# Kernel tuning notes

Hardware: AMD Instinct MI355X
Metric: run time of the kernel (lower is better)

## Reference

```python
import jax, jax.numpy as jnp
import numpy as np

GAMMA = 1.0  # matches init_kwargs gamma
B, N, M = 128, 512, 512


def setup_inputs() -> dict:
    key = jax.random.key(0)
    D = jax.random.uniform(key, (B, N, M), dtype=jnp.float32)
    return {"D": D}


def _softmin3(a, b, c, gamma):
    # soft_min over the 3 DP neighbors: -gamma * logsumexp(-x/gamma)
    z = jnp.stack([a, b, c], axis=0) * (-1.0 / gamma)
    return -gamma * jax.nn.logsumexp(z, axis=0)


def reference(D):
    """Soft-DTW forward: returns R[:, N, M], shape (B,).
    DP over rows (lax.scan), inner scan over columns carries R[i, j-1].
    Vectorized over the batch dimension.
    """
    gamma = GAMMA
    b, n, m = D.shape
    dt = D.dtype
    inf = jnp.array(jnp.inf, dt)

    def row_step(prev_row, d_row):
        # prev_row: (b, m+1) = R[i-1, 0..m]; d_row: (b, m) = D[:, i-1, :]
        def col_step(left, xs):
            diag, up, d = xs  # each (b,)
            new = d + _softmin3(diag, up, left, gamma)
            return new, new
        xs = (prev_row[:, :-1].T, prev_row[:, 1:].T, d_row.T)  # each (m, b)
        _, outs = jax.lax.scan(col_step, jnp.full((b,), inf, dt), xs)
        new_row = jnp.concatenate([jnp.full((b, 1), inf, dt), outs.T], axis=1)
        return new_row, None

    # R[0, :] = [0, inf, inf, ...]
    init = jnp.concatenate([jnp.zeros((b, 1), dt), jnp.full((b, m), inf, dt)], axis=1)
    final_row, _ = jax.lax.scan(row_step, init, jnp.swapaxes(D, 0, 1))  # scan over rows (n, b, m)
    return final_row[:, -1]
```

## Files before the change

kernel.cpp:

```cpp
#include <hip/hip_runtime.h>


#define BB 128
#define NN 512
#define MM 512
#define L2E 1.4426950408889634f
#define LN2 0.6931471805599453f

__device__ __forceinline__ int iclamp(int x, int lo, int hi) {
    return x < lo ? lo : (x > hi ? hi : x);
}

template<int CTRL>
__device__ __forceinline__ float dpp_fmax(float v) {
    const int s = __builtin_amdgcn_update_dpp(
        __float_as_int(v), __float_as_int(v), CTRL, 0xF, 0xF, false);
    return __builtin_fmaxf(v, __int_as_float(s));
}

template<int P, int U, bool JCHK>
__device__ __forceinline__ void dostep(
    const float* __restrict__ Db, const int lane, const int w,
    const int jb, const int sbase, const int tq,
    float (&r1)[2], float (&r2)[2], float2 (&buf)[2][8],
    int& irow, float& sh, float& shprev, float& bl, float& bd,
    float (*hs)[2])
{
    {
        const int r = iclamp(irow, 0, NN - 1);
        buf[P ^ 1][U] = *(const float2*)(Db + ((r << 9) + jb));
        irow += 1;
    }

    float nv1;
    {
        constexpr int par  = (U >= 1) ? P : (P ^ 1);
        constexpr int slot = (U >= 1) ? (U - 1) : 7;
        const float d = buf[par][slot].y;
        float wgt = __builtin_amdgcn_exp2f(-L2E * d);
        if (JCHK) {
            const bool junk = (sbase + (P * 8 + U - 1)) >= tq;
            wgt = junk ? 0.0f : wgt;
        }
        nv1 = wgt * ((r1[1] + r1[0]) + r2[0]);
    }
    if (lane == 63) hs[w][U & 1] = nv1;

    float nv0;
    {
        const float lf = (lane == 0) ? bl : sh;
        const float dg = (lane == 0) ? bd : shprev;
        const float d  = buf[P][U].x;
        float wgt = __builtin_amdgcn_exp2f(-L2E * d);
        if (JCHK) {
            const bool junk = (sbase + (P * 8 + U)) >= tq;
            wgt = junk ? 0.0f : wgt;
        }
        nv0 = wgt * ((r1[0] + lf) + dg);
    }

    r2[0] = r1[0]; r2[1] = r1[1];
    r1[0] = nv0;   r1[1] = nv1;
    bd = bl;

    asm volatile("s_waitcnt lgkmcnt(0)" ::: "memory");
    __builtin_amdgcn_s_barrier();
    asm volatile("" ::: "memory");

    shprev = sh;
    sh = __shfl_up(r1[1], 1, 64);
    if (w > 0) bl = hs[w - 1][U & 1];
}

__device__ __forceinline__ void renorm4(
    const int lane, const int w,
    float (&r1)[2], float (&r2)[2], float& sh, float& shprev,
    float& bl, float& bd, float& gexp, float* mxs)
{
    float m = __builtin_fmaxf(r1[0], r1[1]);
    m = dpp_fmax<0x111>(m);
    m = dpp_fmax<0x112>(m);
    m = dpp_fmax<0x114>(m);
    m = dpp_fmax<0x118>(m);
    m = dpp_fmax<0x142>(m);
    m = dpp_fmax<0x143>(m);
    if (lane == 63) mxs[w] = m;
    asm volatile("s_waitcnt lgkmcnt(0)" ::: "memory");
    __builtin_amdgcn_s_barrier();
    asm volatile("" ::: "memory");
    const float m4 = __builtin_fmaxf(__builtin_fmaxf(mxs[0], mxs[1]),
                                     __builtin_fmaxf(mxs[2], mxs[3]));
    const int eb = (__float_as_int(m4) >> 23) & 255;
    const int ex = (eb > 0 && eb < 255) ? (eb - 127) : 0;
    const float rs = __int_as_float((127 - ex) << 23);
    r1[0] *= rs; r1[1] *= rs; r2[0] *= rs; r2[1] *= rs;
    sh *= rs; shprev *= rs;
    bl *= rs;
    bd *= rs;
    gexp += (float)ex;
}

#define S8(PP, JJ) \
    dostep<PP,0,JJ>(Db,lane,w,jb,sbase,tq,r1,r2,buf,irow,sh,shprev,bl,bd,hs); \
    dostep<PP,1,JJ>(Db,lane,w,jb,sbase,tq,r1,r2,buf,irow,sh,shprev,bl,bd,hs); \
    dostep<PP,2,JJ>(Db,lane,w,jb,sbase,tq,r1,r2,buf,irow,sh,shprev,bl,bd,hs); \
    dostep<PP,3,JJ>(Db,lane,w,jb,sbase,tq,r1,r2,buf,irow,sh,shprev,bl,bd,hs); \
    dostep<PP,4,JJ>(Db,lane,w,jb,sbase,tq,r1,r2,buf,irow,sh,shprev,bl,bd,hs); \
    dostep<PP,5,JJ>(Db,lane,w,jb,sbase,tq,r1,r2,buf,irow,sh,shprev,bl,bd,hs); \
    dostep<PP,6,JJ>(Db,lane,w,jb,sbase,tq,r1,r2,buf,irow,sh,shprev,bl,bd,hs); \
    dostep<PP,7,JJ>(Db,lane,w,jb,sbase,tq,r1,r2,buf,irow,sh,shprev,bl,bd,hs);

__launch_bounds__(256, 1)
__global__ void softdtw_wave4(const float* __restrict__ D, float* __restrict__ out) {
    const int b = blockIdx.x;
    const int tid = (int)threadIdx.x;
    const int w = tid >> 6;
    const int lane = tid & 63;
    const int jb = (w << 7) + (lane << 1);
    const int tq = jb + NN;
    const float* __restrict__ Db = D + (size_t)b * (NN * MM);

    __shared__ float hsS[4][2];
    __shared__ float mxsS[4];
    float (*hs)[2] = hsS;
    float* mxs = mxsS;

    if (tid < 8) ((float*)hsS)[tid] = 0.0f;
    if (tid < 4) mxsS[tid] = 0.0f;
    asm volatile("s_waitcnt lgkmcnt(0)" ::: "memory");
    __builtin_amdgcn_s_barrier();
    asm volatile("" ::: "memory");

    float r1[2] = {0.0f, 0.0f};
    float r2[2] = {0.0f, 0.0f};
    float2 buf[2][8];
    #pragma unroll
    for (int v = 0; v < 8; ++v) buf[1][v] = make_float2(0.0f, 0.0f);
    #pragma unroll
    for (int v = 0; v < 8; ++v) {
        const int r = iclamp(v - jb, 0, NN - 1);
        buf[0][v] = *(const float2*)(Db + ((r << 9) + jb));
    }
    int irow = 8 - jb;
    float sh = 0.0f, shprev = 0.0f;
    float bl = 0.0f;
    float bd = (w == 0) ? 1.0f : 0.0f;
    float gexp = 0.0f;

    #pragma unroll 1
    for (int qq = 0; qq < 32; ++qq) {
        const int sbase = qq << 4;
        renorm4(lane, w, r1, r2, sh, shprev, bl, bd, gexp, mxs);
        S8(0, false)
        S8(1, false)
    }
    #pragma unroll 1
    for (int qq = 32; qq < 63; ++qq) {
        const int sbase = qq << 4;
        renorm4(lane, w, r1, r2, sh, shprev, bl, bd, gexp, mxs);
        S8(0, true)
        S8(1, true)
    }
    {
        const int sbase = 1008;
        renorm4(lane, w, r1, r2, sh, shprev, bl, bd, gexp, mxs);
        S8(0, true)
        dostep<1,0,true>(Db,lane,w,jb,sbase,tq,r1,r2,buf,irow,sh,shprev,bl,bd,hs);
        dostep<1,1,true>(Db,lane,w,jb,sbase,tq,r1,r2,buf,irow,sh,shprev,bl,bd,hs);
        dostep<1,2,true>(Db,lane,w,jb,sbase,tq,r1,r2,buf,irow,sh,shprev,bl,bd,hs);
        dostep<1,3,true>(Db,lane,w,jb,sbase,tq,r1,r2,buf,irow,sh,shprev,bl,bd,hs);
        dostep<1,4,true>(Db,lane,w,jb,sbase,tq,r1,r2,buf,irow,sh,shprev,bl,bd,hs);
        dostep<1,5,true>(Db,lane,w,jb,sbase,tq,r1,r2,buf,irow,sh,shprev,bl,bd,hs);
        dostep<1,6,true>(Db,lane,w,jb,sbase,tq,r1,r2,buf,irow,sh,shprev,bl,bd,hs);
    }

    if (w == 3 && lane == 63) {
        out[b] = -(__builtin_amdgcn_logf(r1[1]) + gexp) * LN2;
    }
}

extern "C" void kernel_launch(void* const* d_in, const int* in_sizes, int n_in,
                              void* d_out, int out_size, void* d_ws, size_t ws_size,
                              hipStream_t stream) {
    const float* D = (const float*)d_in[0];
    float* out = (float*)d_out;
    softdtw_wave4<<<BB, 256, 0, stream>>>(D, out);
}
```

Measured before the change: 395.9 us.

## Skew waves by one block and pass boundary values through LDS ring

Replaces the per-step workgroup barrier with a wave-skewed schedule: each wave runs one 16-step block behind its predecessor, handing boundary values through a 64-entry LDS ring and synchronising only once per block. Renormalisation becomes per-wave (readlane max), and the exponent difference between adjacent waves is exchanged through LDS to rescale incoming boundary values. This removes roughly 16 barriers per block but adds three extra block iterations of pipeline fill/drain, always-on junk masking, and per-wave exponent bookkeeping.

Result: faster. 377.2 us (-4.7%).

```diff
diff --git a/kernel.cpp b/kernel.cpp
--- a/kernel.cpp
+++ b/kernel.cpp
@@ -18,19 +18,20 @@
     return __builtin_fmaxf(v, __int_as_float(s));
 }
 
-template<int P, int U, bool JCHK>
+template<int P, int U>
 __device__ __forceinline__ void dostep(
     const float* __restrict__ Db, const int lane, const int w,
     const int jb, const int sbase, const int tq,
     float (&r1)[2], float (&r2)[2], float2 (&buf)[2][8],
     int& irow, float& sh, float& shprev, float& bl, float& bd,
-    float (*hs)[2])
+    float* ring, const float scale)
 {
     {
         const int r = iclamp(irow, 0, NN - 1);
         buf[P ^ 1][U] = *(const float2*)(Db + ((r << 9) + jb));
         irow += 1;
     }
+    const int s = sbase + P * 8 + U;
 
     float nv1;
     {
@@ -38,13 +39,11 @@
         constexpr int slot = (U >= 1) ? (U - 1) : 7;
         const float d = buf[par][slot].y;
         float wgt = __builtin_amdgcn_exp2f(-L2E * d);
-        if (JCHK) {
-            const bool junk = (sbase + (P * 8 + U - 1)) >= tq;
-            wgt = junk ? 0.0f : wgt;
-        }
+        const bool junk = (s - 1) >= tq;
+        wgt = junk ? 0.0f : wgt;
         nv1 = wgt * ((r1[1] + r1[0]) + r2[0]);
     }
-    if (lane == 63) hs[w][U & 1] = nv1;
+    if (lane == 63 && w < 3) ring[(w << 6) + (s & 63)] = nv1;
 
     float nv0;
     {
@@ -52,30 +51,22 @@
         const float dg = (lane == 0) ? bd : shprev;
         const float d  = buf[P][U].x;
         float wgt = __builtin_amdgcn_exp2f(-L2E * d);
-        if (JCHK) {
-            const bool junk = (sbase + (P * 8 + U)) >= tq;
-            wgt = junk ? 0.0f : wgt;
-        }
+        const bool junk = s >= tq;
+        wgt = junk ? 0.0f : wgt;
         nv0 = wgt * ((r1[0] + lf) + dg);
     }
 
     r2[0] = r1[0]; r2[1] = r1[1];
     r1[0] = nv0;   r1[1] = nv1;
     bd = bl;
-
-    asm volatile("s_waitcnt lgkmcnt(0)" ::: "memory");
-    __builtin_amdgcn_s_barrier();
-    asm volatile("" ::: "memory");
-
     shprev = sh;
     sh = __shfl_up(r1[1], 1, 64);
-    if (w > 0) bl = hs[w - 1][U & 1];
+    if (w > 0) bl = ring[((w - 1) << 6) + (s & 63)] * scale;
 }
 
-__device__ __forceinline__ void renorm4(
-    const int lane, const int w,
+__device__ __forceinline__ void renorm_local(
     float (&r1)[2], float (&r2)[2], float& sh, float& shprev,
-    float& bl, float& bd, float& gexp, float* mxs)
+    float& bl, float& bd, float& gexp)
 {
     float m = __builtin_fmaxf(r1[0], r1[1]);
     m = dpp_fmax<0x111>(m);
@@ -84,13 +75,8 @@
     m = dpp_fmax<0x118>(m);
     m = dpp_fmax<0x142>(m);
     m = dpp_fmax<0x143>(m);
-    if (lane == 63) mxs[w] = m;
-    asm volatile("s_waitcnt lgkmcnt(0)" ::: "memory");
-    __builtin_amdgcn_s_barrier();
-    asm volatile("" ::: "memory");
-    const float m4 = __builtin_fmaxf(__builtin_fmaxf(mxs[0], mxs[1]),
-                                     __builtin_fmaxf(mxs[2], mxs[3]));
-    const int eb = (__float_as_int(m4) >> 23) & 255;
+    const int mb = __builtin_amdgcn_readlane(__float_as_int(m), 63);
+    const int eb = (mb >> 23) & 255;
     const int ex = (eb > 0 && eb < 255) ? (eb - 127) : 0;
     const float rs = __int_as_float((127 - ex) << 23);
     r1[0] *= rs; r1[1] *= rs; r2[0] *= rs; r2[1] *= rs;
@@ -100,18 +86,18 @@
     gexp += (float)ex;
 }
 
-#define S8(PP, JJ) \
-    dostep<PP,0,JJ>(Db,lane,w,jb,sbase,tq,r1,r2,buf,irow,sh,shprev,bl,bd,hs); \
-    dostep<PP,1,JJ>(Db,lane,w,jb,sbase,tq,r1,r2,buf,irow,sh,shprev,bl,bd,hs); \
-    dostep<PP,2,JJ>(Db,lane,w,jb,sbase,tq,r1,r2,buf,irow,sh,shprev,bl,bd,hs); \
-    dostep<PP,3,JJ>(Db,lane,w,jb,sbase,tq,r1,r2,buf,irow,sh,shprev,bl,bd,hs); \
-    dostep<PP,4,JJ>(Db,lane,w,jb,sbase,tq,r1,r2,buf,irow,sh,shprev,bl,bd,hs); \
-    dostep<PP,5,JJ>(Db,lane,w,jb,sbase,tq,r1,r2,buf,irow,sh,shprev,bl,bd,hs); \
-    dostep<PP,6,JJ>(Db,lane,w,jb,sbase,tq,r1,r2,buf,irow,sh,shprev,bl,bd,hs); \
-    dostep<PP,7,JJ>(Db,lane,w,jb,sbase,tq,r1,r2,buf,irow,sh,shprev,bl,bd,hs);
+#define S8(PP) \
+    dostep<PP,0>(Db,lane,w,jb,sbase,tq,r1,r2,buf,irow,sh,shprev,bl,bd,ring,scale); \
+    dostep<PP,1>(Db,lane,w,jb,sbase,tq,r1,r2,buf,irow,sh,shprev,bl,bd,ring,scale); \
+    dostep<PP,2>(Db,lane,w,jb,sbase,tq,r1,r2,buf,irow,sh,shprev,bl,bd,ring,scale); \
+    dostep<PP,3>(Db,lane,w,jb,sbase,tq,r1,r2,buf,irow,sh,shprev,bl,bd,ring,scale); \
+    dostep<PP,4>(Db,lane,w,jb,sbase,tq,r1,r2,buf,irow,sh,shprev,bl,bd,ring,scale); \
+    dostep<PP,5>(Db,lane,w,jb,sbase,tq,r1,r2,buf,irow,sh,shprev,bl,bd,ring,scale); \
+    dostep<PP,6>(Db,lane,w,jb,sbase,tq,r1,r2,buf,irow,sh,shprev,bl,bd,ring,scale); \
+    dostep<PP,7>(Db,lane,w,jb,sbase,tq,r1,r2,buf,irow,sh,shprev,bl,bd,ring,scale);
 
 __launch_bounds__(256, 1)
-__global__ void softdtw_wave4(const float* __restrict__ D, float* __restrict__ out) {
+__global__ void softdtw_skew4(const float* __restrict__ D, float* __restrict__ out) {
     const int b = blockIdx.x;
     const int tid = (int)threadIdx.x;
     const int w = tid >> 6;
@@ -120,16 +106,13 @@
     const int tq = jb + NN;
     const float* __restrict__ Db = D + (size_t)b * (NN * MM);
 
-    __shared__ float hsS[4][2];
-    __shared__ float mxsS[4];
-    float (*hs)[2] = hsS;
-    float* mxs = mxsS;
+    __shared__ float ringS[3 * 64];
+    __shared__ float gxS[8];
+    float* ring = ringS;
+    float* gx = gxS;
 
-    if (tid < 8) ((float*)hsS)[tid] = 0.0f;
-    if (tid < 4) mxsS[tid] = 0.0f;
-    asm volatile("s_waitcnt lgkmcnt(0)" ::: "memory");
-    __builtin_amdgcn_s_barrier();
-    asm volatile("" ::: "memory");
+    if (tid < 3 * 64) ringS[tid] = 0.0f;
+    if (tid < 8) gxS[tid] = 0.0f;
 
     float r1[2] = {0.0f, 0.0f};
     float r2[2] = {0.0f, 0.0f};
@@ -148,30 +131,35 @@
     float gexp = 0.0f;
 
     #pragma unroll 1
-    for (int qq = 0; qq < 32; ++qq) {
-        const int sbase = qq << 4;
-        renorm4(lane, w, r1, r2, sh, shprev, bl, bd, gexp, mxs);
-        S8(0, false)
-        S8(1, false)
-    }
-    #pragma unroll 1
-    for (int qq = 32; qq < 63; ++qq) {
-        const int sbase = qq << 4;
-        renorm4(lane, w, r1, r2, sh, shprev, bl, bd, gexp, mxs);
-        S8(0, true)
-        S8(1, true)
-    }
-    {
-        const int sbase = 1008;
-        renorm4(lane, w, r1, r2, sh, shprev, bl, bd, gexp, mxs);
-        S8(0, true)
-        dostep<1,0,true>(Db,lane,w,jb,sbase,tq,r1,r2,buf,irow,sh,shprev,bl,bd,hs);
-        dostep<1,1,true>(Db,lane,w,jb,sbase,tq,r1,r2,buf,irow,sh,shprev,bl,bd,hs);
-        dostep<1,2,true>(Db,lane,w,jb,sbase,tq,r1,r2,buf,irow,sh,shprev,bl,bd,hs);
-        dostep<1,3,true>(Db,lane,w,jb,sbase,tq,r1,r2,buf,irow,sh,shprev,bl,bd,hs);
-        dostep<1,4,true>(Db,lane,w,jb,sbase,tq,r1,r2,buf,irow,sh,shprev,bl,bd,hs);
-        dostep<1,5,true>(Db,lane,w,jb,sbase,tq,r1,r2,buf,irow,sh,shprev,bl,bd,hs);
-        dostep<1,6,true>(Db,lane,w,jb,sbase,tq,r1,r2,buf,irow,sh,shprev,bl,bd,hs);
+    for (int k = 0; k < 67; ++k) {
+        asm volatile("s_waitcnt lgkmcnt(0)" ::: "memory");
+        __builtin_amdgcn_s_barrier();
+        asm volatile("" ::: "memory");
+        const int kw = k - w;
+        if (kw < 0 || kw > 63) continue;
+        const int sbase = kw << 4;
+        renorm_local(r1, r2, sh, shprev, bl, bd, gexp);
+        if (lane == 63 && w < 3) gx[(w << 1) + (k & 1)] = gexp;
+        float scale = 1.0f;
+        if (w > 0) {
+            const float gxp = gx[((w - 1) << 1) + ((k - 1) & 1)];
+            int dlt = (int)(gxp - gexp);
+            dlt = iclamp(dlt, -126, 126);
+            scale = __int_as_float((127 + dlt) << 23);
+        }
+        if (kw < 63) {
+            S8(0)
+            S8(1)
+        } else {
+            S8(0)
+            dostep<1,0>(Db,lane,w,jb,sbase,tq,r1,r2,buf,irow,sh,shprev,bl,bd,ring,scale);
+            dostep<1,1>(Db,lane,w,jb,sbase,tq,r1,r2,buf,irow,sh,shprev,bl,bd,ring,scale);
+            dostep<1,2>(Db,lane,w,jb,sbase,tq,r1,r2,buf,irow,sh,shprev,bl,bd,ring,scale);
+            dostep<1,3>(Db,lane,w,jb,sbase,tq,r1,r2,buf,irow,sh,shprev,bl,bd,ring,scale);
+            dostep<1,4>(Db,lane,w,jb,sbase,tq,r1,r2,buf,irow,sh,shprev,bl,bd,ring,scale);
+            dostep<1,5>(Db,lane,w,jb,sbase,tq,r1,r2,buf,irow,sh,shprev,bl,bd,ring,scale);
+            dostep<1,6>(Db,lane,w,jb,sbase,tq,r1,r2,buf,irow,sh,shprev,bl,bd,ring,scale);
+        }
     }
 
     if (w == 3 && lane == 63) {
@@ -184,5 +172,5 @@
                               hipStream_t stream) {
     const float* D = (const float*)d_in[0];
     float* out = (float*)d_out;
-    softdtw_wave4<<<BB, 256, 0, stream>>>(D, out);
+    softdtw_skew4<<<BB, 256, 0, stream>>>(D, out);
 }
```
